# Kernel tuning notes

Hardware: AMD Instinct MI355X
Metric: run time of the kernel (lower is better)

Reference implementation:

```python
import jax, jax.numpy as jnp
import numpy as np

ALPHA = 0.2  # LeakyReLU slope
BN_EPS = 1e-5


def _conv_circ(x, w, b, pad_w):
    # circular padding only on width (torch padding=(0, pad_w), padding_mode='circular')
    x = jnp.pad(x, ((0, 0), (0, 0), (0, 0), (pad_w, pad_w)), mode='wrap')
    y = jax.lax.conv_general_dilated(x, w, window_strides=(1, 1), padding='VALID',
                                     dimension_numbers=('NCHW', 'OIHW', 'NCHW'))
    return y + b[None, :, None, None]


def _graph_conv(x, n, w, b, pad_w):
    h1 = _conv_circ(x, w, b, pad_w)  # [B, N, C, F]
    h2 = _conv_circ(n, w, b, pad_w)
    B, N, C, F = h1.shape
    h1f = h1.reshape(B, N, C * F)
    h2f = h2.reshape(B, N, C * F)
    a = jnp.einsum('bnf,bmf->bnm', h1f, h2f)          # [B, N, N]
    a = jnp.where(a > 0, a, ALPHA * a)                 # LeakyReLU
    att = jax.nn.softmax(a, axis=1)                    # torch Softmax(dim=1)
    return (att @ h1f).reshape(B, N, C, F)


def _bn_pool_relu(x, gamma, beta, mean, var):
    # eval-mode BatchNorm2d -> MaxPool2d((1,2)) -> ReLU
    inv = gamma / jnp.sqrt(var + BN_EPS)
    x = x * inv[None, :, None, None] + (beta - mean * inv)[None, :, None, None]
    W = x.shape[-1]
    W2 = (W // 2) * 2
    x = x[..., :W2].reshape(*x.shape[:-1], W2 // 2, 2).max(axis=-1)
    return jax.nn.relu(x)


def setup_inputs() -> dict:
    key = jax.random.key(0)
    ks = jax.random.split(key, 16)
    B = 16384
    return {
        'x': jax.random.normal(ks[0], (B, 5, 5, 50), jnp.float32),
        'conv1_w': jax.random.normal(ks[1], (32, 5, 5, 11), jnp.float32) * 0.1,
        'conv1_b': jax.random.normal(ks[2], (32,), jnp.float32) * 0.1,
        'bn1_gamma': jax.random.uniform(ks[3], (32,), jnp.float32, 0.5, 1.5),
        'bn1_beta': jax.random.normal(ks[4], (32,), jnp.float32) * 0.1,
        'bn1_mean': jax.random.normal(ks[5], (32,), jnp.float32) * 0.1,
        'bn1_var': jax.random.uniform(ks[6], (32,), jnp.float32, 0.5, 1.5),
        'conv2_w': jax.random.normal(ks[7], (32, 32, 1, 5), jnp.float32) * 0.1,
        'conv2_b': jax.random.normal(ks[8], (32,), jnp.float32) * 0.1,
        'bn2_gamma': jax.random.uniform(ks[9], (32,), jnp.float32, 0.5, 1.5),
        'bn2_beta': jax.random.normal(ks[10], (32,), jnp.float32) * 0.1,
        'bn2_mean': jax.random.normal(ks[11], (32,), jnp.float32) * 0.1,
        'bn2_var': jax.random.uniform(ks[12], (32,), jnp.float32, 0.5, 1.5),
        'lin_w': jax.random.normal(ks[13], (13, 384), jnp.float32) * 0.05,
        'lin_b': jax.random.normal(ks[14], (13,), jnp.float32) * 0.05,
    }


def reference(x, conv1_w, conv1_b, bn1_gamma, bn1_beta, bn1_mean, bn1_var,
              conv2_w, conv2_b, bn2_gamma, bn2_beta, bn2_mean, bn2_var,
              lin_w, lin_b):
    W = x.shape[-1]
    xa, na = x[..., :W // 2], x[..., W // 2:]
    xa = _graph_conv(xa, xa, conv1_w, conv1_b, 5)
    na = _graph_conv(na, na, conv1_w, conv1_b, 5)
    xa = _bn_pool_relu(xa, bn1_gamma, bn1_beta, bn1_mean, bn1_var)
    na = _bn_pool_relu(na, bn1_gamma, bn1_beta, bn1_mean, bn1_var)
    x2 = _graph_conv(xa, na, conv2_w, conv2_b, 2)
    n2 = _graph_conv(na, xa, conv2_w, conv2_b, 2)
    x2 = _bn_pool_relu(x2, bn2_gamma, bn2_beta, bn2_mean, bn2_var)
    n2 = _bn_pool_relu(n2, bn2_gamma, bn2_beta, bn2_mean, bn2_var)
    flat = jnp.concatenate([x2, n2], axis=-1).reshape(x.shape[0], -1)  # [B, 384]
    # Dropout(0.2) is identity in eval mode
    return flat @ lin_w.T + lin_b
```

## Files before the change

### kernel.cpp

```cpp
#include <hip/hip_runtime.h>
#include <math.h>

#define ALPHA 0.2f
#define BN_EPS 1e-5f

typedef __attribute__((ext_vector_type(8))) short short8;
typedef __attribute__((ext_vector_type(4))) float v4f;

__device__ __forceinline__ unsigned short f2bf_rne(float f) {
    union { float f; unsigned u; } x; x.f = f;
    unsigned r = x.u + 0x7FFFu + ((x.u >> 16) & 1u);
    return (unsigned short)(r >> 16);
}
__device__ __forceinline__ float bf2f(unsigned short h) {
    union { float f; unsigned u; } x; x.u = ((unsigned)h) << 16;
    return x.f;
}
__device__ __forceinline__ unsigned cvtpk_bf16(float a0, float a1) {
    unsigned r;
    asm("v_cvt_pk_bf16_f32 %0, %1, %2" : "=v"(r) : "v"(a0), "v"(a1));
    return r;
}
__device__ __forceinline__ void hilo_pair(float a0, float a1, unsigned& hp, unsigned& lp) {
    hp = cvtpk_bf16(a0, a1);
    union { unsigned u; float f; } c0, c1;
    c0.u = hp << 16; c1.u = hp & 0xFFFF0000u;
    lp = cvtpk_bf16(a0 - c0.f, a1 - c1.f);
}

__global__ __launch_bounds__(256) void prep_kernel(const float* __restrict__ w1,
                                                   const float* __restrict__ w2,
                                                   unsigned short* __restrict__ ws16) {
    int s = blockIdx.x * 256 + threadIdx.x;
    if (s < 1408) {
        int lane = s & 63;
        int ktnt = s >> 6;
        int kw = ktnt >> 1;
        int nt = ktnt & 1;
        int oc = nt * 16 + (lane & 15);
        int quad = lane >> 4;
        for (int j = 0; j < 8; ++j) {
            int k = quad * 8 + j;
            float w = (k < 25) ? w1[oc * 275 + k * 11 + kw] : 0.f;
            unsigned short h = f2bf_rne(w);
            ws16[s * 8 + j] = h;
            ws16[11264 + s * 8 + j] = f2bf_rne(w - bf2f(h));
        }
    } else if (s < 2048) {
        int s2 = s - 1408;
        int lane = s2 & 63;
        int ktnt = s2 >> 6;
        int kw = ktnt >> 1;
        int nt = ktnt & 1;
        int oc = nt * 16 + (lane & 15);
        int quad = lane >> 4;
        for (int j = 0; j < 8; ++j) {
            int ic = quad * 8 + j;
            float w = w2[oc * 160 + ic * 5 + kw];
            unsigned short h = f2bf_rne(w);
            ws16[22528 + s2 * 8 + j] = h;
            ws16[27648 + s2 * 8 + j] = f2bf_rne(w - bf2f(h));
        }
    }
}

#define IT 2984
#define HLO 858
#define XKT 860
#define CSTO 5968
#define LDS_TOTAL (5968 + 128)

__global__ __launch_bounds__(256, 6) void gcn_kernel(
    const float* __restrict__ x,
    const float* __restrict__ w1, const float* __restrict__ b1,
    const float* __restrict__ g1, const float* __restrict__ be1,
    const float* __restrict__ mu1, const float* __restrict__ va1,
    const float* __restrict__ w2, const float* __restrict__ b2,
    const float* __restrict__ g2, const float* __restrict__ be2,
    const float* __restrict__ mu2, const float* __restrict__ va2,
    const float* __restrict__ lw, const float* __restrict__ lb,
    const unsigned short* __restrict__ ws16,
    float* __restrict__ out)
{
    __shared__ __align__(16) float lds[LDS_TOTAL];
    float* cst = lds + CSTO;

    const int tid = threadIdx.x;
    const int b0  = blockIdx.x * 2;

    if (tid < 250) {
        int rowid = tid / 5;
        int s = tid - rowid * 5;
        int it = (rowid >= 25) ? 1 : 0;
        int k = rowid - it * 25;
        const float2* src = (const float2*)(x + (size_t)b0 * 1250) + it * 625 + k * 25 + s * 5;
        unsigned short* XU = (unsigned short*)(lds + it * IT + XKT);
#pragma unroll
        for (int e = 0; e < 5; ++e) {
            float2 v = src[e];
            int w50 = s * 10 + 2 * e;
            {
                int half = (w50 >= 25) ? 1 : 0;
                int w = w50 - half * 25;
                unsigned short u = f2bf_rne(v.x);
                int a = half * 1400 + (w + 5) * 40 + k;
                XU[a] = u;
                if (w >= 20) XU[a - 1000] = u;
                if (w <= 4)  XU[a + 1000] = u;
            }
            {
                int w51 = w50 + 1;
                int half = (w51 >= 25) ? 1 : 0;
                int w = w51 - half * 25;
                unsigned short u = f2bf_rne(v.y);
                int a = half * 1400 + (w + 5) * 40 + k;
                XU[a] = u;
                if (w >= 20) XU[a - 1000] = u;
                if (w <= 4)  XU[a + 1000] = u;
            }
        }
    }
    if (tid < 140) {
        int it = (tid >= 70) ? 1 : 0;
        int r2 = tid - it * 70;
        int half = (r2 >= 35) ? 1 : 0;
        int w3 = r2 - half * 35;
        int a = half * 1400 + w3 * 40;
        unsigned short* XU = (unsigned short*)(lds + it * IT + XKT);
        XU[a + 25] = 0;
        unsigned* XD = (unsigned*)XU;
        XD[(a >> 1) + 13] = 0;
        XD[(a >> 1) + 14] = 0;
        XD[(a >> 1) + 15] = 0;
    }
    if (tid < 64) {
        int oc = tid & 31;
        if (tid < 32) {
            float inv = g1[oc] * rsqrtf(va1[oc] + BN_EPS);
            cst[oc]      = inv;
            cst[32 + oc] = be1[oc] - mu1[oc] * inv;
        } else {
            float inv = g2[oc] * rsqrtf(va2[oc] + BN_EPS);
            cst[64 + oc] = inv;
            cst[96 + oc] = be2[oc] - mu2[oc] * inv;
        }
    }
    __syncthreads();

    {
        const int wave = tid >> 6, lane = tid & 63;
        const int it = wave >> 1;
        const int Mtb = (wave & 1) * 2;
        const int quad = lane >> 4, m16 = lane & 15;
        const unsigned* XK = (const unsigned*)(lds + it * IT + XKT);

        int ab[2];
#pragma unroll
        for (int mt = 0; mt < 2; ++mt) {
            int mg = (Mtb + mt) * 16 + m16;
            int half = mg >> 5, pos = mg & 31;
            pos = (pos > 24) ? 24 : pos;
            ab[mt] = half * 700 + pos * 20 + quad * 4;
        }

        v4f zz = {0.f, 0.f, 0.f, 0.f};
        v4f acc[2][2];
        acc[0][0] = zz; acc[0][1] = zz; acc[1][0] = zz; acc[1][1] = zz;

        for (int kw = 0; kw < 11; ++kw) {
            short8 a0 = *(const short8*)(XK + ab[0] + kw * 20);
            short8 a1 = *(const short8*)(XK + ab[1] + kw * 20);
#pragma unroll
            for (int nt = 0; nt < 2; ++nt) {
                const short8* ph = (const short8*)(ws16 + ((kw * 2 + nt) * 64 + lane) * 8);
                const short8* pl = (const short8*)(ws16 + 11264 + ((kw * 2 + nt) * 64 + lane) * 8);
                short8 bh = *ph;
                short8 bl = *pl;
                acc[0][nt] = __builtin_amdgcn_mfma_f32_16x16x32_bf16(a0, bh, acc[0][nt], 0, 0, 0);
                acc[0][nt] = __builtin_amdgcn_mfma_f32_16x16x32_bf16(a0, bl, acc[0][nt], 0, 0, 0);
                acc[1][nt] = __builtin_amdgcn_mfma_f32_16x16x32_bf16(a1, bh, acc[1][nt], 0, 0, 0);
                acc[1][nt] = __builtin_amdgcn_mfma_f32_16x16x32_bf16(a1, bl, acc[1][nt], 0, 0, 0);
            }
        }

        __syncthreads();

        float biasv0 = b1[m16], biasv1 = b1[16 + m16];
        unsigned* HD = (unsigned*)(lds + it * IT);
#pragma unroll
        for (int mt = 0; mt < 2; ++mt) {
#pragma unroll
            for (int rr = 0; rr < 2; ++rr) {
                int mg0 = (Mtb + mt) * 16 + quad * 4 + rr * 2;
                int half = mg0 >> 5, pos0 = mg0 & 31;
                if (pos0 <= 24) {
                    int kd = pos0 >> 1;
#pragma unroll
                    for (int nt = 0; nt < 2; ++nt) {
                        float bias = nt ? biasv1 : biasv0;
                        float v0 = acc[mt][nt][rr * 2] + bias;
                        float v1 = acc[mt][nt][rr * 2 + 1] + bias;
                        unsigned hp, lp;
                        hilo_pair(v0, v1, hp, lp);
                        int ch = half * 32 + nt * 16 + m16;
                        HD[kd * 66 + ch] = hp;
                        HD[858 + kd * 66 + ch] = lp;
                    }
                }
            }
        }
    }
    __syncthreads();

    {
        const int wave = tid >> 6, lane = tid & 63;
        const int it = wave >> 1, half = wave & 1;
        const int m16 = lane & 15, q = lane >> 4;
        const unsigned* D = (const unsigned*)(lds + it * IT);
        short8 fh[2], fl[2];
#pragma unroll
        for (int t = 0; t < 2; ++t) {
            int row = half * 32 + t * 16 + m16;
            union { unsigned u[4]; short8 v; } H, L;
#pragma unroll
            for (int i = 0; i < 4; ++i) {
                int k0 = q * 8 + 2 * i;
                unsigned mh = D[(k0 >> 1) * 66 + row];
                unsigned ml = D[858 + (k0 >> 1) * 66 + row];
                if (k0 == 24) { mh &= 0xFFFFu; ml &= 0xFFFFu; }
                if (k0 > 24)  { mh = 0u; ml = 0u; }
                H.u[i] = mh; L.u[i] = ml;
            }
            fh[t] = H.v; fl[t] = L.v;
        }
        v4f zz = {0.f, 0.f, 0.f, 0.f};
        v4f acc[2][2];
        acc[0][0] = zz; acc[0][1] = zz; acc[1][0] = zz; acc[1][1] = zz;
#pragma unroll
        for (int mt = 0; mt < 2; ++mt)
#pragma unroll
            for (int nt = 0; nt < 2; ++nt) {
                acc[mt][nt] = __builtin_amdgcn_mfma_f32_16x16x32_bf16(fh[mt], fh[nt], acc[mt][nt], 0, 0, 0);
                acc[mt][nt] = __builtin_amdgcn_mfma_f32_16x16x32_bf16(fh[mt], fl[nt], acc[mt][nt], 0, 0, 0);
                acc[mt][nt] = __builtin_amdgcn_mfma_f32_16x16x32_bf16(fl[mt], fh[nt], acc[mt][nt], 0, 0, 0);
            }
        __syncthreads();
        float* A = &lds[it * IT + HLO];
#pragma unroll
        for (int mt = 0; mt < 2; ++mt)
#pragma unroll
            for (int nt = 0; nt < 2; ++nt)
#pragma unroll
                for (int r = 0; r < 4; ++r) {
                    int m = mt * 16 + q * 4 + r;
                    int n = nt * 16 + m16;
                    float s = acc[mt][nt][r];
                    s = (s > 0.f) ? s : ALPHA * s;
                    A[(half * 32 + m) * 33 + n] = s;
                }
    }
    __syncthreads();

    {
        int row = tid >> 1, q = tid & 1;
        int it = row >> 6, rm = row & 63;
        float* rp = &lds[it * IT + HLO + rm * 33];
        float ev[16];
        float mx = -INFINITY;
#pragma unroll
        for (int k = 0; k < 16; ++k) { ev[k] = rp[q + 2 * k]; mx = fmaxf(mx, ev[k]); }
        mx = fmaxf(mx, __shfl_xor(mx, 1));
        float s = 0.f;
#pragma unroll
        for (int k = 0; k < 16; ++k) { ev[k] = __expf(ev[k] - mx); s += ev[k]; }
        s += __shfl_xor(s, 1);
        float inv = 1.f / s;
#pragma unroll
        for (int k = 0; k < 16; ++k) rp[q + 2 * k] = ev[k] * inv;
    }
    __syncthreads();

    {
        const int wave = tid >> 6, lane = tid & 63;
        const int it = wave >> 1, half = wave & 1;
        const int m16 = lane & 15, q = lane >> 4;
        const unsigned short* U = (const unsigned short*)(lds + it * IT);
        const float* AT = &lds[it * IT + HLO];

        short8 ah[2];
#pragma unroll
        for (int mt = 0; mt < 2; ++mt) {
            int pos = mt * 16 + m16;
            int kd = pos >> 1, par = pos & 1;
            union { unsigned u[4]; short8 v; } H;
#pragma unroll
            for (int i = 0; i < 4; ++i) {
                int ch = half * 32 + q * 8 + 2 * i;
                unsigned h0 = U[kd * 132 + ch * 2 + par];
                unsigned h1u = U[kd * 132 + (ch + 1) * 2 + par];
                H.u[i] = h0 | (h1u << 16);
            }
            ah[mt] = H.v;
        }
        short8 bh[2], bl[2];
#pragma unroll
        for (int nt = 0; nt < 2; ++nt) {
            union { unsigned u[4]; short8 v; } H, L;
#pragma unroll
            for (int i = 0; i < 4; ++i) {
                int m = q * 8 + 2 * i;
                float a0 = AT[(half * 32 + m) * 33 + nt * 16 + m16];
                float a1 = AT[(half * 32 + m + 1) * 33 + nt * 16 + m16];
                unsigned hp, lp;
                hilo_pair(a0, a1, hp, lp);
                H.u[i] = hp; L.u[i] = lp;
            }
            bh[nt] = H.v; bl[nt] = L.v;
        }
        v4f zz = {0.f, 0.f, 0.f, 0.f};
        v4f acc[2][2];
        acc[0][0] = zz; acc[0][1] = zz; acc[1][0] = zz; acc[1][1] = zz;
#pragma unroll
        for (int mt = 0; mt < 2; ++mt)
#pragma unroll
            for (int nt = 0; nt < 2; ++nt) {
                acc[mt][nt] = __builtin_amdgcn_mfma_f32_16x16x32_bf16(ah[mt], bh[nt], acc[mt][nt], 0, 0, 0);
                acc[mt][nt] = __builtin_amdgcn_mfma_f32_16x16x32_bf16(ah[mt], bl[nt], acc[mt][nt], 0, 0, 0);
            }

        __syncthreads();

        unsigned short* PT = (unsigned short*)(lds + it * IT) + half * 832;
#pragma unroll
        for (int mt = 0; mt < 2; ++mt)
#pragma unroll
            for (int nt = 0; nt < 2; ++nt) {
                int n = nt * 16 + m16;
                float inv = cst[n], sh = cst[32 + n];
#pragma unroll
                for (int rr = 0; rr < 2; ++rr) {
                    int pos0 = mt * 16 + q * 4 + rr * 2;
                    if (pos0 < 24) {
                        float v0 = acc[mt][nt][rr * 2] * inv + sh;
                        float v1 = acc[mt][nt][rr * 2 + 1] * inv + sh;
                        float p = fmaxf(fmaxf(v0, v1), 0.f);
                        int j = pos0 >> 1;
                        unsigned short h = f2bf_rne(p);
                        PT[(n >> 1) * 26 + j * 2 + (n & 1)] = h;
                        PT[416 + (n >> 1) * 26 + j * 2 + (n & 1)] = f2bf_rne(p - bf2f(h));
                    }
                }
            }
    }
    __syncthreads();

    {
        const int wave = tid >> 6, lane = tid & 63;
        const int it = wave >> 1, half = wave & 1;
        const int m16 = lane & 15, q = lane >> 4;
        const unsigned* PTD = (const unsigned*)(lds + it * IT) + half * 416;

        v4f zz = {0.f, 0.f, 0.f, 0.f};
        v4f acc[2]; acc[0] = zz; acc[1] = zz;
#pragma unroll
        for (int kw = 0; kw < 5; ++kw) {
            int owr = m16 + kw - 2;
            if (owr < 0) owr += 12;
            if (owr >= 12) owr -= 12;
            union { unsigned u[4]; short8 v; } H, L;
#pragma unroll
            for (int i = 0; i < 4; ++i) {
                H.u[i] = PTD[(q * 4 + i) * 13 + owr];
                L.u[i] = PTD[208 + (q * 4 + i) * 13 + owr];
            }
#pragma unroll
            for (int nt = 0; nt < 2; ++nt) {
                const short8* ph = (const short8*)(ws16 + 22528 + ((kw * 2 + nt) * 64 + lane) * 8);
                const short8* pl = (const short8*)(ws16 + 27648 + ((kw * 2 + nt) * 64 + lane) * 8);
                short8 wbh = *ph, wbl = *pl;
                acc[nt] = __builtin_amdgcn_mfma_f32_16x16x32_bf16(H.v, wbh, acc[nt], 0, 0, 0);
                acc[nt] = __builtin_amdgcn_mfma_f32_16x16x32_bf16(H.v, wbl, acc[nt], 0, 0, 0);
                acc[nt] = __builtin_amdgcn_mfma_f32_16x16x32_bf16(L.v, wbh, acc[nt], 0, 0, 0);
            }
        }

        __syncthreads();

        if (q < 3) {
            unsigned* H2 = (unsigned*)(lds + it * IT);
#pragma unroll
            for (int nt = 0; nt < 2; ++nt) {
                float bias = b2[nt * 16 + m16];
                int ch = half * 32 + nt * 16 + m16;
#pragma unroll
                for (int rr = 0; rr < 2; ++rr) {
                    float v0 = acc[nt][rr * 2] + bias;
                    float v1 = acc[nt][rr * 2 + 1] + bias;
                    unsigned hp, lp;
                    hilo_pair(v0, v1, hp, lp);
                    H2[(q * 2 + rr) * 66 + ch] = hp;
                    H2[396 + (q * 2 + rr) * 66 + ch] = lp;
                }
            }
        }
    }
    __syncthreads();

    {
        const int wave = tid >> 6, lane = tid & 63;
        const int it = wave >> 1, half = wave & 1;
        const int m16 = lane & 15, q = lane >> 4;
        const unsigned* D = (const unsigned*)(lds + it * IT);
        short8 ah[2], al[2], bh[2], bl[2];
#pragma unroll
        for (int t = 0; t < 2; ++t) {
            int rowA = (1 - half) * 32 + t * 16 + m16;
            int rowB = half * 32 + t * 16 + m16;
            union { unsigned u[4]; short8 v; } HA, LA, HB, LB;
#pragma unroll
            for (int i = 0; i < 4; ++i) {
                int k0 = q * 8 + 2 * i;
                unsigned a_h = D[(k0 >> 1) * 66 + rowA];
                unsigned a_l = D[396 + (k0 >> 1) * 66 + rowA];
                unsigned b_h = D[(k0 >> 1) * 66 + rowB];
                unsigned b_l = D[396 + (k0 >> 1) * 66 + rowB];
                if (k0 > 10) { a_h = 0u; a_l = 0u; b_h = 0u; b_l = 0u; }
                HA.u[i] = a_h; LA.u[i] = a_l; HB.u[i] = b_h; LB.u[i] = b_l;
            }
            ah[t] = HA.v; al[t] = LA.v; bh[t] = HB.v; bl[t] = LB.v;
        }
        v4f zz = {0.f, 0.f, 0.f, 0.f};
        v4f acc[2][2];
        acc[0][0] = zz; acc[0][1] = zz; acc[1][0] = zz; acc[1][1] = zz;
#pragma unroll
        for (int mt = 0; mt < 2; ++mt)
#pragma unroll
            for (int nt = 0; nt < 2; ++nt) {
                acc[mt][nt] = __builtin_amdgcn_mfma_f32_16x16x32_bf16(ah[mt], bh[nt], acc[mt][nt], 0, 0, 0);
                acc[mt][nt] = __builtin_amdgcn_mfma_f32_16x16x32_bf16(ah[mt], bl[nt], acc[mt][nt], 0, 0, 0);
                acc[mt][nt] = __builtin_amdgcn_mfma_f32_16x16x32_bf16(al[mt], bh[nt], acc[mt][nt], 0, 0, 0);
            }
        float* A = &lds[it * IT + HLO];
#pragma unroll
        for (int mt = 0; mt < 2; ++mt)
#pragma unroll
            for (int nt = 0; nt < 2; ++nt)
#pragma unroll
                for (int r = 0; r < 4; ++r) {
                    int m = mt * 16 + q * 4 + r;
                    int n = nt * 16 + m16;
                    float s = acc[mt][nt][r];
                    s = (s > 0.f) ? s : ALPHA * s;
                    A[(half * 32 + m) * 33 + n] = s;
                }
    }
    __syncthreads();

    {
        int row = tid >> 1, q = tid & 1;
        int it = row >> 6, rm = row & 63;
        float* rp = &lds[it * IT + HLO + rm * 33];
        float ev[16];
        float mx = -INFINITY;
#pragma unroll
        for (int k = 0; k < 16; ++k) { ev[k] = rp[q + 2 * k]; mx = fmaxf(mx, ev[k]); }
        mx = fmaxf(mx, __shfl_xor(mx, 1));
        float s = 0.f;
#pragma unroll
        for (int k = 0; k < 16; ++k) { ev[k] = __expf(ev[k] - mx); s += ev[k]; }
        s += __shfl_xor(s, 1);
        float inv = 1.f / s;
#pragma unroll
        for (int k = 0; k < 16; ++k) rp[q + 2 * k] = ev[k] * inv;
    }
    __syncthreads();

    {
        const int wave = tid >> 6, lane = tid & 63;
        const int it = wave >> 1, half = wave & 1;
        const int m16 = lane & 15, q = lane >> 4;
        const unsigned short* U = (const unsigned short*)(lds + it * IT);
        const float* AT = &lds[it * IT + HLO];

        int kd = m16 >> 1, par = m16 & 1;
        union { unsigned u[4]; short8 v; } HA, LA;
#pragma unroll
        for (int i = 0; i < 4; ++i) {
            int ch = half * 32 + q * 8 + 2 * i;
            unsigned h0 = U[kd * 132 + ch * 2 + par];
            unsigned h1u = U[kd * 132 + (ch + 1) * 2 + par];
            unsigned l0 = U[792 + kd * 132 + ch * 2 + par];
            unsigned l1 = U[792 + kd * 132 + (ch + 1) * 2 + par];
            HA.u[i] = h0 | (h1u << 16);
            LA.u[i] = l0 | (l1 << 16);
        }
        short8 bh[2], bl[2];
#pragma unroll
        for (int nt = 0; nt < 2; ++nt) {
            union { unsigned u[4]; short8 v; } H, L;
#pragma unroll
            for (int i = 0; i < 4; ++i) {
                int m = q * 8 + 2 * i;
                float a0 = AT[(half * 32 + m) * 33 + nt * 16 + m16];
                float a1 = AT[(half * 32 + m + 1) * 33 + nt * 16 + m16];
                unsigned hp, lp;
                hilo_pair(a0, a1, hp, lp);
                H.u[i] = hp; L.u[i] = lp;
            }
            bh[nt] = H.v; bl[nt] = L.v;
        }
        v4f zz = {0.f, 0.f, 0.f, 0.f};
        v4f acc[2]; acc[0] = zz; acc[1] = zz;
#pragma unroll
        for (int nt = 0; nt < 2; ++nt) {
            acc[nt] = __builtin_amdgcn_mfma_f32_16x16x32_bf16(HA.v, bh[nt], acc[nt], 0, 0, 0);
            acc[nt] = __builtin_amdgcn_mfma_f32_16x16x32_bf16(HA.v, bl[nt], acc[nt], 0, 0, 0);
            acc[nt] = __builtin_amdgcn_mfma_f32_16x16x32_bf16(LA.v, bh[nt], acc[nt], 0, 0, 0);
        }

        __syncthreads();

        if (q < 3) {
#pragma unroll
            for (int nt = 0; nt < 2; ++nt) {
                int n = nt * 16 + m16;
                float inv = cst[64 + n], sh = cst[96 + n];
#pragma unroll
                for (int rr = 0; rr < 2; ++rr) {
                    int j = q * 2 + rr;
                    float v0 = acc[nt][rr * 2] * inv + sh;
                    float v1 = acc[nt][rr * 2 + 1] * inv + sh;
                    lds[it * IT + n * 12 + half * 6 + j] =
                        fmaxf(fmaxf(v0, v1), 0.f);
                }
            }
        }
    }
    __syncthreads();

    if (tid < 208) {
        int s8 = tid & 7;
        int rest = tid >> 3;
        int it = (rest >= 13) ? 1 : 0;
        int o = rest - it * 13;
        const float4* wv4 = (const float4*)(lw + o * 384 + s8 * 48);
        const float4* fv4 = (const float4*)&lds[it * IT + s8 * 48];
        float s = 0.f;
#pragma unroll
        for (int i = 0; i < 12; ++i) {
            float4 w4 = wv4[i];
            float4 f4 = fv4[i];
            s += f4.x * w4.x + f4.y * w4.y + f4.z * w4.z + f4.w * w4.w;
        }
        s += __shfl_down(s, 4, 8);
        s += __shfl_down(s, 2, 8);
        s += __shfl_down(s, 1, 8);
        if (s8 == 0) out[(size_t)(b0 + it) * 13 + o] = s + lb[o];
    }
}

extern "C" void kernel_launch(void* const* d_in, const int* in_sizes, int n_in,
                              void* d_out, int out_size, void* d_ws, size_t ws_size,
                              hipStream_t stream) {
    const float* x   = (const float*)d_in[0];
    const float* w1  = (const float*)d_in[1];
    const float* b1  = (const float*)d_in[2];
    const float* g1  = (const float*)d_in[3];
    const float* be1 = (const float*)d_in[4];
    const float* mu1 = (const float*)d_in[5];
    const float* va1 = (const float*)d_in[6];
    const float* w2  = (const float*)d_in[7];
    const float* b2  = (const float*)d_in[8];
    const float* g2  = (const float*)d_in[9];
    const float* be2 = (const float*)d_in[10];
    const float* mu2 = (const float*)d_in[11];
    const float* va2 = (const float*)d_in[12];
    const float* lw  = (const float*)d_in[13];
    const float* lb  = (const float*)d_in[14];
    float* out = (float*)d_out;
    unsigned short* ws16 = (unsigned short*)d_ws;

    prep_kernel<<<8, 256, 0, stream>>>(w1, w2, ws16);

    int B = in_sizes[0] / 1250;
    gcn_kernel<<<B / 2, 256, 0, stream>>>(x, w1, b1, g1, be1, mu1, va1,
                                          w2, b2, g2, be2, mu2, va2, lw, lb,
                                          ws16, out);
}
```

Measured before the change: 245.6 us.

## Fuse softmax into score MFMA registers and store attention as packed bf16

Computes LeakyReLU and the softmax directly on the MFMA accumulators, using cross-lane shuffles for the max and sum, instead of writing fp32 scores to LDS and running a separate softmax pass. The normalized attention is stored as packed bf16 pairs, which removes one barrier and one LDS round trip and drops the low-part correction MFMAs on the attention operand. The smaller LDS footprint allows raising launch bounds to 8 blocks per CU. The cost is reduced precision, since attention weights are now bf16-only with no hi/lo split, which may hurt accuracy.

```diff
diff --git a/kernel.cpp b/kernel.cpp
--- a/kernel.cpp
+++ b/kernel.cpp
@@ -64,13 +64,13 @@
     }
 }
 
-#define IT 2984
+#define IT 2264
 #define HLO 858
 #define XKT 860
-#define CSTO 5968
-#define LDS_TOTAL (5968 + 128)
-
-__global__ __launch_bounds__(256, 6) void gcn_kernel(
+#define CSTO 4528
+#define LDS_TOTAL (4528 + 128)
+
+__global__ __launch_bounds__(256, 8) void gcn_kernel(
     const float* __restrict__ x,
     const float* __restrict__ w1, const float* __restrict__ b1,
     const float* __restrict__ g1, const float* __restrict__ be1,
@@ -244,39 +244,49 @@
                 acc[mt][nt] = __builtin_amdgcn_mfma_f32_16x16x32_bf16(fh[mt], fl[nt], acc[mt][nt], 0, 0, 0);
                 acc[mt][nt] = __builtin_amdgcn_mfma_f32_16x16x32_bf16(fl[mt], fh[nt], acc[mt][nt], 0, 0, 0);
             }
+#pragma unroll
+        for (int mt = 0; mt < 2; ++mt)
+#pragma unroll
+            for (int nt = 0; nt < 2; ++nt)
+#pragma unroll
+                for (int r = 0; r < 4; ++r) {
+                    float s = acc[mt][nt][r];
+                    acc[mt][nt][r] = (s > 0.f) ? s : ALPHA * s;
+                }
+        float invs[2][4];
+#pragma unroll
+        for (int mt = 0; mt < 2; ++mt)
+#pragma unroll
+            for (int r = 0; r < 4; ++r) {
+                float m2 = fmaxf(acc[mt][0][r], acc[mt][1][r]);
+                m2 = fmaxf(m2, __shfl_xor(m2, 1));
+                m2 = fmaxf(m2, __shfl_xor(m2, 2));
+                m2 = fmaxf(m2, __shfl_xor(m2, 4));
+                m2 = fmaxf(m2, __shfl_xor(m2, 8));
+                float e0 = __expf(acc[mt][0][r] - m2);
+                float e1 = __expf(acc[mt][1][r] - m2);
+                acc[mt][0][r] = e0; acc[mt][1][r] = e1;
+                float sm = e0 + e1;
+                sm += __shfl_xor(sm, 1);
+                sm += __shfl_xor(sm, 2);
+                sm += __shfl_xor(sm, 4);
+                sm += __shfl_xor(sm, 8);
+                invs[mt][r] = 1.f / sm;
+            }
         __syncthreads();
-        float* A = &lds[it * IT + HLO];
-#pragma unroll
-        for (int mt = 0; mt < 2; ++mt)
-#pragma unroll
-            for (int nt = 0; nt < 2; ++nt)
-#pragma unroll
-                for (int r = 0; r < 4; ++r) {
-                    int m = mt * 16 + q * 4 + r;
-                    int n = nt * 16 + m16;
-                    float s = acc[mt][nt][r];
-                    s = (s > 0.f) ? s : ALPHA * s;
-                    A[(half * 32 + m) * 33 + n] = s;
-                }
-    }
-    __syncthreads();
-
-    {
-        int row = tid >> 1, q = tid & 1;
-        int it = row >> 6, rm = row & 63;
-        float* rp = &lds[it * IT + HLO + rm * 33];
-        float ev[16];
-        float mx = -INFINITY;
-#pragma unroll
-        for (int k = 0; k < 16; ++k) { ev[k] = rp[q + 2 * k]; mx = fmaxf(mx, ev[k]); }
-        mx = fmaxf(mx, __shfl_xor(mx, 1));
-        float s = 0.f;
-#pragma unroll
-        for (int k = 0; k < 16; ++k) { ev[k] = __expf(ev[k] - mx); s += ev[k]; }
-        s += __shfl_xor(s, 1);
-        float inv = 1.f / s;
-#pragma unroll
-        for (int k = 0; k < 16; ++k) rp[q + 2 * k] = ev[k] * inv;
+        unsigned* ATB = (unsigned*)(lds + it * IT) + HLO + half * 544;
+#pragma unroll
+        for (int mt = 0; mt < 2; ++mt)
+#pragma unroll
+            for (int rr = 0; rr < 2; ++rr) {
+                int md = 8 * mt + 2 * q + rr;
+#pragma unroll
+                for (int nt = 0; nt < 2; ++nt) {
+                    float a0 = acc[mt][nt][rr * 2]     * invs[mt][rr * 2];
+                    float a1 = acc[mt][nt][rr * 2 + 1] * invs[mt][rr * 2 + 1];
+                    ATB[md * 34 + nt * 16 + m16] = cvtpk_bf16(a0, a1);
+                }
+            }
     }
     __syncthreads();
 
@@ -285,7 +295,7 @@
         const int it = wave >> 1, half = wave & 1;
         const int m16 = lane & 15, q = lane >> 4;
         const unsigned short* U = (const unsigned short*)(lds + it * IT);
-        const float* AT = &lds[it * IT + HLO];
+        const unsigned* ATB = (const unsigned*)(lds + it * IT) + HLO + half * 544;
 
         short8 ah[2];
 #pragma unroll
@@ -302,20 +312,14 @@
             }
             ah[mt] = H.v;
         }
-        short8 bh[2], bl[2];
+        short8 bh[2];
 #pragma unroll
         for (int nt = 0; nt < 2; ++nt) {
-            union { unsigned u[4]; short8 v; } H, L;
-#pragma unroll
-            for (int i = 0; i < 4; ++i) {
-                int m = q * 8 + 2 * i;
-                float a0 = AT[(half * 32 + m) * 33 + nt * 16 + m16];
-                float a1 = AT[(half * 32 + m + 1) * 33 + nt * 16 + m16];
-                unsigned hp, lp;
-                hilo_pair(a0, a1, hp, lp);
-                H.u[i] = hp; L.u[i] = lp;
-            }
-            bh[nt] = H.v; bl[nt] = L.v;
+            union { unsigned u[4]; short8 v; } H;
+#pragma unroll
+            for (int i = 0; i < 4; ++i)
+                H.u[i] = ATB[(q * 4 + i) * 34 + nt * 16 + m16];
+            bh[nt] = H.v;
         }
         v4f zz = {0.f, 0.f, 0.f, 0.f};
         v4f acc[2][2];
@@ -323,10 +327,8 @@
 #pragma unroll
         for (int mt = 0; mt < 2; ++mt)
 #pragma unroll
-            for (int nt = 0; nt < 2; ++nt) {
+            for (int nt = 0; nt < 2; ++nt)
                 acc[mt][nt] = __builtin_amdgcn_mfma_f32_16x16x32_bf16(ah[mt], bh[nt], acc[mt][nt], 0, 0, 0);
-                acc[mt][nt] = __builtin_amdgcn_mfma_f32_16x16x32_bf16(ah[mt], bl[nt], acc[mt][nt], 0, 0, 0);
-            }
 
         __syncthreads();
 
@@ -440,38 +442,48 @@
                 acc[mt][nt] = __builtin_amdgcn_mfma_f32_16x16x32_bf16(ah[mt], bl[nt], acc[mt][nt], 0, 0, 0);
                 acc[mt][nt] = __builtin_amdgcn_mfma_f32_16x16x32_bf16(al[mt], bh[nt], acc[mt][nt], 0, 0, 0);
             }
-        float* A = &lds[it * IT + HLO];
 #pragma unroll
         for (int mt = 0; mt < 2; ++mt)
 #pragma unroll
             for (int nt = 0; nt < 2; ++nt)
 #pragma unroll
                 for (int r = 0; r < 4; ++r) {
-                    int m = mt * 16 + q * 4 + r;
-                    int n = nt * 16 + m16;
                     float s = acc[mt][nt][r];
-                    s = (s > 0.f) ? s : ALPHA * s;
-                    A[(half * 32 + m) * 33 + n] = s;
-                }
-    }
-    __syncthreads();
-
-    {
-        int row = tid >> 1, q = tid & 1;
-        int it = row >> 6, rm = row & 63;
-        float* rp = &lds[it * IT + HLO + rm * 33];
-        float ev[16];
-        float mx = -INFINITY;
-#pragma unroll
-        for (int k = 0; k < 16; ++k) { ev[k] = rp[q + 2 * k]; mx = fmaxf(mx, ev[k]); }
-        mx = fmaxf(mx, __shfl_xor(mx, 1));
-        float s = 0.f;
-#pragma unroll
-        for (int k = 0; k < 16; ++k) { ev[k] = __expf(ev[k] - mx); s += ev[k]; }
-        s += __shfl_xor(s, 1);
-        float inv = 1.f / s;
-#pragma unroll
-        for (int k = 0; k < 16; ++k) rp[q + 2 * k] = ev[k] * inv;
+                    acc[mt][nt][r] = (s > 0.f) ? s : ALPHA * s;
+                }
+        float invs[2][4];
+#pragma unroll
+        for (int mt = 0; mt < 2; ++mt)
+#pragma unroll
+            for (int r = 0; r < 4; ++r) {
+                float m2 = fmaxf(acc[mt][0][r], acc[mt][1][r]);
+                m2 = fmaxf(m2, __shfl_xor(m2, 1));
+                m2 = fmaxf(m2, __shfl_xor(m2, 2));
+                m2 = fmaxf(m2, __shfl_xor(m2, 4));
+                m2 = fmaxf(m2, __shfl_xor(m2, 8));
+                float e0 = __expf(acc[mt][0][r] - m2);
+                float e1 = __expf(acc[mt][1][r] - m2);
+                acc[mt][0][r] = e0; acc[mt][1][r] = e1;
+                float sm = e0 + e1;
+                sm += __shfl_xor(sm, 1);
+                sm += __shfl_xor(sm, 2);
+                sm += __shfl_xor(sm, 4);
+                sm += __shfl_xor(sm, 8);
+                invs[mt][r] = 1.f / sm;
+            }
+        unsigned* ATB = (unsigned*)(lds + it * IT) + HLO + half * 544;
+#pragma unroll
+        for (int mt = 0; mt < 2; ++mt)
+#pragma unroll
+            for (int rr = 0; rr < 2; ++rr) {
+                int md = 8 * mt + 2 * q + rr;
+#pragma unroll
+                for (int nt = 0; nt < 2; ++nt) {
+                    float a0 = acc[mt][nt][rr * 2]     * invs[mt][rr * 2];
+                    float a1 = acc[mt][nt][rr * 2 + 1] * invs[mt][rr * 2 + 1];
+                    ATB[md * 34 + nt * 16 + m16] = cvtpk_bf16(a0, a1);
+                }
+            }
     }
     __syncthreads();
 
@@ -480,7 +492,7 @@
         const int it = wave >> 1, half = wave & 1;
         const int m16 = lane & 15, q = lane >> 4;
         const unsigned short* U = (const unsigned short*)(lds + it * IT);
-        const float* AT = &lds[it * IT + HLO];
+        const unsigned* ATB = (const unsigned*)(lds + it * IT) + HLO + half * 544;
 
         int kd = m16 >> 1, par = m16 & 1;
         union { unsigned u[4]; short8 v; } HA, LA;
@@ -494,27 +506,20 @@
             HA.u[i] = h0 | (h1u << 16);
             LA.u[i] = l0 | (l1 << 16);
         }
-        short8 bh[2], bl[2];
+        short8 bh[2];
 #pragma unroll
         for (int nt = 0; nt < 2; ++nt) {
-            union { unsigned u[4]; short8 v; } H, L;
-#pragma unroll
-            for (int i = 0; i < 4; ++i) {
-                int m = q * 8 + 2 * i;
-                float a0 = AT[(half * 32 + m) * 33 + nt * 16 + m16];
-                float a1 = AT[(half * 32 + m + 1) * 33 + nt * 16 + m16];
-                unsigned hp, lp;
-                hilo_pair(a0, a1, hp, lp);
-                H.u[i] = hp; L.u[i] = lp;
-            }
-            bh[nt] = H.v; bl[nt] = L.v;
+            union { unsigned u[4]; short8 v; } H;
+#pragma unroll
+            for (int i = 0; i < 4; ++i)
+                H.u[i] = ATB[(q * 4 + i) * 34 + nt * 16 + m16];
+            bh[nt] = H.v;
         }
         v4f zz = {0.f, 0.f, 0.f, 0.f};
         v4f acc[2]; acc[0] = zz; acc[1] = zz;
 #pragma unroll
         for (int nt = 0; nt < 2; ++nt) {
             acc[nt] = __builtin_amdgcn_mfma_f32_16x16x32_bf16(HA.v, bh[nt], acc[nt], 0, 0, 0);
-            acc[nt] = __builtin_amdgcn_mfma_f32_16x16x32_bf16(HA.v, bl[nt], acc[nt], 0, 0, 0);
             acc[nt] = __builtin_amdgcn_mfma_f32_16x16x32_bf16(LA.v, bh[nt], acc[nt], 0, 0, 0);
         }
 
```

Result: slower. 285.3 us (+16.2%).
